# Kernel tuning notes

Measured on AMD Instinct MI355X. Metric: run time of the kernel, lower is better.

## Reference

```python
import jax, jax.numpy as jnp
import numpy as np

NUM_SLOTS = 4096
NUM_CLUSTER = 10
SLOT_DIM = 64
EPS = 1e-8
N_ITER = 3
LN_EPS = 1e-5


def _ln(x, g, b):
    m = jnp.mean(x, axis=-1, keepdims=True)
    v = jnp.var(x, axis=-1, keepdims=True)
    return (x - m) / jnp.sqrt(v + LN_EPS) * g + b


def setup_inputs() -> dict:
    key = jax.random.key(0)
    ks = jax.random.split(key, 24)
    d, S = SLOT_DIM, NUM_SLOTS
    s = d ** -0.5
    f32 = jnp.float32
    return {
        "cluster_centers": jax.random.normal(ks[0], (NUM_CLUSTER, d), f32),
        "Wk": jax.random.normal(ks[1], (d, d), f32) * s,
        "bk": jnp.zeros((d,), f32),
        "Wq": jax.random.normal(ks[2], (d, d), f32) * s,
        "bq": jnp.zeros((d,), f32),
        "Wv": jax.random.normal(ks[3], (d, d), f32) * s,
        "bv": jnp.zeros((d,), f32),
        "cc_g": jnp.ones((d,), f32),
        "cc_b": jnp.zeros((d,), f32),
        "W_ih": jax.random.normal(ks[4], (3 * d, d), f32) * s,
        "W_hh": jax.random.normal(ks[5], (3 * d, d), f32) * s,
        "b_ih": jnp.zeros((3 * d,), f32),
        "b_hh": jnp.zeros((3 * d,), f32),
        "ln_g": jnp.ones((d,), f32),
        "ln_b": jnp.zeros((d,), f32),
        "W1": jax.random.normal(ks[6], (2 * d, d), f32) * s,
        "b1": jnp.zeros((2 * d,), f32),
        "W2": jax.random.normal(ks[7], (d, 2 * d), f32) * (2 * d) ** -0.5,
        "b2": jnp.zeros((d,), f32),
        "Wa": jax.random.normal(ks[8], (S, d, d), f32) * s,
        "ba": jnp.zeros((S, d), f32),
        "Wb": jax.random.normal(ks[9], (S, d, d), f32) * s,
        "bb": jnp.zeros((S, d), f32),
    }


def reference(cluster_centers, Wk, bk, Wq, bq, Wv, bv, cc_g, cc_b,
              W_ih, W_hh, b_ih, b_hh, ln_g, ln_b, W1, b1, W2, b2,
              Wa, ba, Wb, bb):
    temp = SLOT_DIM ** -0.5
    k = cluster_centers @ Wk.T + bk          # [N, d]
    v = cluster_centers @ Wv.T + bv          # [N, d]
    cc = cluster_centers
    for _ in range(N_ITER):
        cc_prev = cc
        q = _ln(cc, cc_g, cc_b) @ Wq.T + bq  # [N, d]
        attn = jnp.einsum('nd,md->nm', k, q) * temp
        attn = jax.nn.softmax(attn, axis=0) + EPS
        attn = attn / jnp.sum(attn, axis=-1, keepdims=True)
        updates = attn @ v                   # [N, d]
        # PyTorch GRUCell
        gi = updates @ W_ih.T + b_ih
        gh = cc_prev @ W_hh.T + b_hh
        ir, iz, inn = jnp.split(gi, 3, axis=-1)
        hr, hz, hn = jnp.split(gh, 3, axis=-1)
        r = jax.nn.sigmoid(ir + hr)
        z = jax.nn.sigmoid(iz + hz)
        n = jnp.tanh(inn + r * hn)
        cc = (1.0 - z) * n + z * cc_prev
        # residual MLP
        h = _ln(cc, ln_g, ln_b)
        cc = cc + jax.nn.relu(h @ W1.T + b1) @ W2.T + b2
    # per-slot 2-layer MLP + max over the 10 clusters, vectorized over slots
    h = jax.nn.relu(jnp.einsum('sij,nj->sni', Wa, cc) + ba[:, None, :])  # [S, N, d]
    out = jnp.einsum('sij,snj->sni', Wb, h) + bb[:, None, :]             # [S, N, d]
    return jnp.max(out, axis=1)                                          # [S, d]
```

## Files before the change

### kernel.cpp

```cpp
#include <hip/hip_runtime.h>
#include <math.h>

#define NCLU 10
#define D    64
#define NSLOT 4096

typedef unsigned int   u32;
typedef unsigned short u16;

typedef __attribute__((ext_vector_type(8))) short  bf16x8;
typedef __attribute__((ext_vector_type(4))) float  f32x4;

__device__ __forceinline__ u16 f2bf_rne(float f) {
    u32 u = __float_as_uint(f);
    return (u16)((u + 0x7fffu + ((u >> 16) & 1u)) >> 16);
}

__device__ __forceinline__ bf16x8 pack8(float4 a, float4 b) {
    bf16x8 r;
    r[0] = (short)f2bf_rne(a.x); r[1] = (short)f2bf_rne(a.y);
    r[2] = (short)f2bf_rne(a.z); r[3] = (short)f2bf_rne(a.w);
    r[4] = (short)f2bf_rne(b.x); r[5] = (short)f2bf_rne(b.y);
    r[6] = (short)f2bf_rne(b.z); r[7] = (short)f2bf_rne(b.w);
    return r;
}

__device__ __forceinline__ float wred(float v) {
#pragma unroll
    for (int off = 32; off > 0; off >>= 1) v += __shfl_xor(v, off);
    return v;
}

__device__ __forceinline__ void load_afrags64(bf16x8 a[4][2], const float* __restrict__ W,
                                              int lc, int quad) {
#pragma unroll
    for (int mt = 0; mt < 4; ++mt)
#pragma unroll
        for (int kt = 0; kt < 2; ++kt) {
            const float* p = W + (16 * mt + lc) * 64 + kt * 32 + quad * 8;
            a[mt][kt] = pack8(*(const float4*)p, *(const float4*)(p + 4));
        }
}

__device__ __forceinline__ void load_afrags128(bf16x8 a[4][2], const float* __restrict__ W,
                                               int ktbase, int lc, int quad) {
#pragma unroll
    for (int mt = 0; mt < 4; ++mt)
#pragma unroll
        for (int kt = 0; kt < 2; ++kt) {
            const float* p = W + (16 * mt + lc) * 128 + (ktbase + kt) * 32 + quad * 8;
            a[mt][kt] = pack8(*(const float4*)p, *(const float4*)(p + 4));
        }
}

__device__ __forceinline__ bf16x8 bfrag(const float* __restrict__ xbase, int xstride,
                                        int lc, int quad, int ktglob) {
    if (lc < NCLU) {
        const float* p = xbase + lc * xstride + ktglob * 32 + quad * 8;
        return pack8(*(const float4*)p, *(const float4*)(p + 4));
    }
    bf16x8 z;
#pragma unroll
    for (int j = 0; j < 8; ++j) z[j] = 0;
    return z;
}

__device__ __forceinline__ void mm_apply(const bf16x8 a[4][2], const float* __restrict__ xbase,
                                         int xstride, int ktbase,
                                         float* __restrict__ obase, int ostride, int ooff,
                                         const float* __restrict__ bias, bool do_relu,
                                         int lc, int quad) {
    f32x4 acc[4];
#pragma unroll
    for (int mt = 0; mt < 4; ++mt) acc[mt] = (f32x4){0.f, 0.f, 0.f, 0.f};
#pragma unroll
    for (int kt = 0; kt < 2; ++kt) {
        bf16x8 b = bfrag(xbase, xstride, lc, quad, ktbase + kt);
#pragma unroll
        for (int mt = 0; mt < 4; ++mt)
            acc[mt] = __builtin_amdgcn_mfma_f32_16x16x32_bf16(a[mt][kt], b, acc[mt], 0, 0, 0);
    }
    if (lc < NCLU) {
#pragma unroll
        for (int mt = 0; mt < 4; ++mt) {
            float4 o;
            o.x = acc[mt][0]; o.y = acc[mt][1]; o.z = acc[mt][2]; o.w = acc[mt][3];
            if (bias) {
                float4 bv = *(const float4*)(bias + 16 * mt + 4 * quad);
                o.x += bv.x; o.y += bv.y; o.z += bv.z; o.w += bv.w;
            }
            if (do_relu) {
                o.x = fmaxf(o.x, 0.f); o.y = fmaxf(o.y, 0.f);
                o.z = fmaxf(o.z, 0.f); o.w = fmaxf(o.w, 0.f);
            }
            *(float4*)(obase + lc * ostride + ooff + 16 * mt + 4 * quad) = o;
        }
    }
}

__global__ __launch_bounds__(640, 3) void phase1_kernel(
    const float* __restrict__ cc0,
    const float* __restrict__ Wk, const float* __restrict__ bk,
    const float* __restrict__ Wq, const float* __restrict__ bq,
    const float* __restrict__ Wv, const float* __restrict__ bv,
    const float* __restrict__ cc_g, const float* __restrict__ cc_b,
    const float* __restrict__ W_ih, const float* __restrict__ W_hh,
    const float* __restrict__ b_ih, const float* __restrict__ b_hh,
    const float* __restrict__ ln_g, const float* __restrict__ ln_b,
    const float* __restrict__ W1, const float* __restrict__ b1,
    const float* __restrict__ W2, const float* __restrict__ b2,
    float* __restrict__ cc_out)
{
    const int t = threadIdx.x;
    const int w = t >> 6;
    const int i = t & 63;
    const int quad = i >> 4;
    const int lc   = i & 15;

    __shared__ float ccl[NCLU][68];
    __shared__ float xl[NCLU][68];
    __shared__ float kl[NCLU][68];
    __shared__ float vl[NCLU][68];
    __shared__ float ql[NCLU][68];
    __shared__ float ul[NCLU][68];
    __shared__ float hl[NCLU][68];
    __shared__ float dl9[NCLU][68];
    __shared__ float dl8[NCLU][68];
    __shared__ float tl[NCLU][132];
    __shared__ float gl[6][NCLU][68];
    __shared__ float al[NCLU][12];

    const float g_cc = cc_g[i], b_cc = cc_b[i];
    const float g_ln = ln_g[i], b_ln = ln_b[i];

    bf16x8 afrA[4][2], afrB[4][2];
#pragma unroll
    for (int mt = 0; mt < 4; ++mt)
#pragma unroll
        for (int kt = 0; kt < 2; ++kt) {
#pragma unroll
            for (int j = 0; j < 8; ++j) { afrA[mt][kt][j] = 0; afrB[mt][kt][j] = 0; }
        }

    const float* biasA = nullptr;
    if (w == 0)      { load_afrags64(afrA, Wq, lc, quad);                    biasA = bq; }
    else if (w <= 3) { load_afrags64(afrA, W_ih + (w - 1) * 64 * 64, lc, quad); biasA = b_ih + (w - 1) * 64; }
    else if (w <= 6) { load_afrags64(afrA, W_hh + (w - 4) * 64 * 64, lc, quad); biasA = b_hh + (w - 4) * 64; }
    else if (w == 7) { load_afrags64(afrA, Wk, lc, quad); }
    else if (w == 8) { load_afrags64(afrA, Wv, lc, quad);
                       load_afrags128(afrB, W2, 2, lc, quad); }
    else             { load_afrags128(afrA, W2, 0, lc, quad); biasA = b2; }

    float c = cc0[w * 64 + i];
    ccl[w][i] = c;
    __syncthreads();

    if (w == 7)      mm_apply(afrA, &ccl[0][0], 68, 0, &kl[0][0], 68, 0, bk, false, lc, quad);
    else if (w == 8) mm_apply(afrA, &ccl[0][0], 68, 0, &vl[0][0], 68, 0, bv, false, lc, quad);
    __syncthreads();

    if (w == 7)      { load_afrags64(afrA, W1, lc, quad);            biasA = b1; }
    else if (w == 8) { load_afrags64(afrA, W1 + 64 * 64, lc, quad);  biasA = b1 + 64; }

    for (int it = 0; it < 3; ++it) {
        {
            float s1 = wred(c), s2 = wred(c * c);
            float mu = s1 * (1.f / 64.f);
            float va = s2 * (1.f / 64.f) - mu * mu;
            xl[w][i] = (c - mu) * rsqrtf(va + 1e-5f) * g_cc + b_cc;
        }
        __syncthreads();

        if (w == 0)
            mm_apply(afrA, &xl[0][0], 68, 0, &ql[0][0], 68, 0, biasA, false, lc, quad);
        else if (w >= 4 && w <= 6)
            mm_apply(afrA, &ccl[0][0], 68, 0, &gl[w - 1][0][0], 68, 0, biasA, false, lc, quad);
        __syncthreads();

        if (i < NCLU) {
            const float4* kf = (const float4*)&kl[w][0];
            const float4* qf = (const float4*)&ql[i][0];
            float a0 = 0.f, a1 = 0.f, a2 = 0.f, a3 = 0.f;
#pragma unroll
            for (int jj = 0; jj < 16; ++jj) {
                float4 kv = kf[jj], qv = qf[jj];
                a0 += kv.x * qv.x; a1 += kv.y * qv.y; a2 += kv.z * qv.z; a3 += kv.w * qv.w;
            }
            al[w][i] = ((a0 + a1) + (a2 + a3)) * 0.125f;
        }
        __syncthreads();

        if (t < NCLU) {
            float mx = -1e30f;
#pragma unroll
            for (int nn = 0; nn < NCLU; ++nn) mx = fmaxf(mx, al[nn][t]);
            float e[NCLU]; float s = 0.f;
#pragma unroll
            for (int nn = 0; nn < NCLU; ++nn) { e[nn] = __expf(al[nn][t] - mx); s += e[nn]; }
            float inv = 1.f / s;
#pragma unroll
            for (int nn = 0; nn < NCLU; ++nn) al[nn][t] = e[nn] * inv + 1e-8f;
        }
        __syncthreads();
        if (t < NCLU) {
            float s = 0.f;
#pragma unroll
            for (int m = 0; m < NCLU; ++m) s += al[t][m];
            float inv = 1.f / s;
#pragma unroll
            for (int m = 0; m < NCLU; ++m) al[t][m] *= inv;
        }
        __syncthreads();

        {
            float u = 0.f;
#pragma unroll
            for (int m = 0; m < NCLU; ++m) u += al[w][m] * vl[m][i];
            ul[w][i] = u;
        }
        __syncthreads();

        if (w >= 1 && w <= 3)
            mm_apply(afrA, &ul[0][0], 68, 0, &gl[w - 1][0][0], 68, 0, biasA, false, lc, quad);
        __syncthreads();

        {
            float ir = gl[0][w][i], iz = gl[1][w][i], inn = gl[2][w][i];
            float hr = gl[3][w][i], hz = gl[4][w][i], hn = gl[5][w][i];
            float r = 1.f / (1.f + __expf(-(ir + hr)));
            float z = 1.f / (1.f + __expf(-(iz + hz)));
            float nn2 = tanhf(inn + r * hn);
            c = (1.f - z) * nn2 + z * c;

            float s1 = wred(c), s2 = wred(c * c);
            float mu = s1 * (1.f / 64.f);
            float va = s2 * (1.f / 64.f) - mu * mu;
            hl[w][i] = (c - mu) * rsqrtf(va + 1e-5f) * g_ln + b_ln;
        }
        __syncthreads();

        if (w == 7)
            mm_apply(afrA, &hl[0][0], 68, 0, &tl[0][0], 132, 0, biasA, true, lc, quad);
        else if (w == 8)
            mm_apply(afrA, &hl[0][0], 68, 0, &tl[0][0], 132, 64, biasA, true, lc, quad);
        __syncthreads();

        if (w == 9)
            mm_apply(afrA, &tl[0][0], 132, 0, &dl9[0][0], 68, 0, biasA, false, lc, quad);
        else if (w == 8)
            mm_apply(afrB, &tl[0][0], 132, 2, &dl8[0][0], 68, 0, nullptr, false, lc, quad);
        __syncthreads();

        c += dl9[w][i] + dl8[w][i];
        ccl[w][i] = c;
        __syncthreads();
    }

    cc_out[w * 64 + i] = c;
}

#define HSTR 72
__global__ __launch_bounds__(64, 4) void phase2_kernel(
    const float* __restrict__ Wa, const float* __restrict__ ba,
    const float* __restrict__ Wb, const float* __restrict__ bb,
    const float* __restrict__ cc, float* __restrict__ out)
{
    const int s = blockIdx.x;
    const int l = threadIdx.x;
    const int quad = l >> 4;
    const int lc   = l & 15;

    __shared__ u16 hT[16 * HSTR];

    const float* wa = Wa + (size_t)s * 4096;
    const float* wb = Wb + (size_t)s * 4096;

    bf16x8 bcc[2];
#pragma unroll
    for (int kt = 0; kt < 2; ++kt) {
        if (lc < NCLU) {
            const float* cp = cc + lc * 64 + kt * 32 + quad * 8;
            bcc[kt] = pack8(*(const float4*)cp, *(const float4*)(cp + 4));
        } else {
#pragma unroll
            for (int j = 0; j < 8; ++j) bcc[kt][j] = 0;
        }
    }

    float4 rg[16];
#pragma unroll
    for (int mt = 0; mt < 4; ++mt)
#pragma unroll
        for (int kt = 0; kt < 2; ++kt) {
            const float* p = wa + (16 * mt + lc) * 64 + kt * 32 + quad * 8;
            rg[(mt * 2 + kt) * 2 + 0] = *(const float4*)p;
            rg[(mt * 2 + kt) * 2 + 1] = *(const float4*)(p + 4);
        }

    bf16x8 frA[4][2];
#pragma unroll
    for (int mt = 0; mt < 4; ++mt)
#pragma unroll
        for (int kt = 0; kt < 2; ++kt)
            frA[mt][kt] = pack8(rg[(mt * 2 + kt) * 2], rg[(mt * 2 + kt) * 2 + 1]);

#pragma unroll
    for (int mt = 0; mt < 4; ++mt)
#pragma unroll
        for (int kt = 0; kt < 2; ++kt) {
            const float* p = wb + (16 * mt + lc) * 64 + kt * 32 + quad * 8;
            rg[(mt * 2 + kt) * 2 + 0] = *(const float4*)p;
            rg[(mt * 2 + kt) * 2 + 1] = *(const float4*)(p + 4);
        }

    f32x4 acc[4];
#pragma unroll
    for (int mt = 0; mt < 4; ++mt) acc[mt] = (f32x4){0.f, 0.f, 0.f, 0.f};
#pragma unroll
    for (int kt = 0; kt < 2; ++kt)
#pragma unroll
        for (int mt = 0; mt < 4; ++mt)
            acc[mt] = __builtin_amdgcn_mfma_f32_16x16x32_bf16(frA[mt][kt], bcc[kt], acc[mt], 0, 0, 0);

#pragma unroll
    for (int mt = 0; mt < 4; ++mt) {
        float4 bav = *(const float4*)(ba + s * 64 + 16 * mt + quad * 4);
        u16 h0 = f2bf_rne(fmaxf(acc[mt][0] + bav.x, 0.f));
        u16 h1 = f2bf_rne(fmaxf(acc[mt][1] + bav.y, 0.f));
        u16 h2 = f2bf_rne(fmaxf(acc[mt][2] + bav.z, 0.f));
        u16 h3 = f2bf_rne(fmaxf(acc[mt][3] + bav.w, 0.f));
        uint2 pk; pk.x = (u32)h0 | ((u32)h1 << 16); pk.y = (u32)h2 | ((u32)h3 << 16);
        *(uint2*)(&hT[lc * HSTR + 16 * mt + quad * 4]) = pk;
    }

    bf16x8 frB[4][2];
#pragma unroll
    for (int mt = 0; mt < 4; ++mt)
#pragma unroll
        for (int kt = 0; kt < 2; ++kt)
            frB[mt][kt] = pack8(rg[(mt * 2 + kt) * 2], rg[(mt * 2 + kt) * 2 + 1]);

    bf16x8 bh[2];
#pragma unroll
    for (int kt = 0; kt < 2; ++kt)
        bh[kt] = *(const bf16x8*)(&hT[lc * HSTR + kt * 32 + quad * 8]);

    f32x4 acc2[4];
#pragma unroll
    for (int mt = 0; mt < 4; ++mt) acc2[mt] = (f32x4){0.f, 0.f, 0.f, 0.f};
#pragma unroll
    for (int kt = 0; kt < 2; ++kt)
#pragma unroll
        for (int mt = 0; mt < 4; ++mt)
            acc2[mt] = __builtin_amdgcn_mfma_f32_16x16x32_bf16(frB[mt][kt], bh[kt], acc2[mt], 0, 0, 0);

    const float NEG = -3.0e38f;
#pragma unroll
    for (int mt = 0; mt < 4; ++mt) {
#pragma unroll
        for (int r = 0; r < 4; ++r) {
            float v = (lc < NCLU) ? acc2[mt][r] : NEG;
#pragma unroll
            for (int off = 1; off < 16; off <<= 1)
                v = fmaxf(v, __shfl_xor(v, off));
            acc2[mt][r] = v;
        }
    }

    if (lc < 4) {
#pragma unroll
        for (int mt = 0; mt < 4; ++mt) {
            int row = 16 * mt + 4 * quad + lc;
            out[s * 64 + row] = acc2[mt][lc] + bb[s * 64 + row];
        }
    }
}

extern "C" void kernel_launch(void* const* d_in, const int* in_sizes, int n_in,
                              void* d_out, int out_size, void* d_ws, size_t ws_size,
                              hipStream_t stream) {
    const float* cc0  = (const float*)d_in[0];
    const float* Wk   = (const float*)d_in[1];
    const float* bk   = (const float*)d_in[2];
    const float* Wq   = (const float*)d_in[3];
    const float* bq   = (const float*)d_in[4];
    const float* Wv   = (const float*)d_in[5];
    const float* bv   = (const float*)d_in[6];
    const float* ccg  = (const float*)d_in[7];
    const float* ccb  = (const float*)d_in[8];
    const float* Wih  = (const float*)d_in[9];
    const float* Whh  = (const float*)d_in[10];
    const float* bih  = (const float*)d_in[11];
    const float* bhh  = (const float*)d_in[12];
    const float* lng  = (const float*)d_in[13];
    const float* lnb  = (const float*)d_in[14];
    const float* W1   = (const float*)d_in[15];
    const float* b1   = (const float*)d_in[16];
    const float* W2   = (const float*)d_in[17];
    const float* b2   = (const float*)d_in[18];
    const float* Wa   = (const float*)d_in[19];
    const float* ba   = (const float*)d_in[20];
    const float* Wb   = (const float*)d_in[21];
    const float* bb   = (const float*)d_in[22];

    float* cc_ws = (float*)d_ws;
    float* out   = (float*)d_out;

    hipLaunchKernelGGL(phase1_kernel, dim3(1), dim3(640), 0, stream,
                       cc0, Wk, bk, Wq, bq, Wv, bv, ccg, ccb,
                       Wih, Whh, bih, bhh, lng, lnb, W1, b1, W2, b2, cc_ws);

    hipLaunchKernelGGL(phase2_kernel, dim3(NSLOT), dim3(64), 0, stream,
                       Wa, ba, Wb, bb, cc_ws, out);
}
```

Baseline: 216.8 us.

## Pack four slots per block and issue all weight loads before conversion

The phase2 kernel now runs four waves per block, one slot each, with a private shared-memory tile per wave, so the grid shrinks to a quarter of its former block count. The Wa, Wb and bias loads are all issued up front into separate register arrays before any bf16 packing, so more global memory traffic is in flight per wave. The cost is higher register pressure (32 float4 staging registers), which may limit occupancy under the new launch bounds.

Measured after the change: 218.5 us. Within noise of the previous version (+0.8%).

```diff
diff --git a/kernel.cpp b/kernel.cpp
--- a/kernel.cpp
+++ b/kernel.cpp
@@ -260,17 +260,19 @@
 }
 
 #define HSTR 72
-__global__ __launch_bounds__(64, 4) void phase2_kernel(
+#define SLOTS_PER_BLK 4
+__global__ __launch_bounds__(256, 4) void phase2_kernel(
     const float* __restrict__ Wa, const float* __restrict__ ba,
     const float* __restrict__ Wb, const float* __restrict__ bb,
     const float* __restrict__ cc, float* __restrict__ out)
 {
-    const int s = blockIdx.x;
-    const int l = threadIdx.x;
+    const int w = threadIdx.x >> 6;
+    const int l = threadIdx.x & 63;
+    const int s = blockIdx.x * SLOTS_PER_BLK + w;
     const int quad = l >> 4;
     const int lc   = l & 15;
 
-    __shared__ u16 hT[16 * HSTR];
+    __shared__ u16 hT[SLOTS_PER_BLK][16 * HSTR];
 
     const float* wa = Wa + (size_t)s * 4096;
     const float* wb = Wb + (size_t)s * 4096;
@@ -287,31 +289,37 @@
         }
     }
 
-    float4 rg[16];
+    float4 bav[4];
+#pragma unroll
+    for (int mt = 0; mt < 4; ++mt)
+        bav[mt] = *(const float4*)(ba + s * 64 + 16 * mt + quad * 4);
+
+    float4 rgA[16];
 #pragma unroll
     for (int mt = 0; mt < 4; ++mt)
 #pragma unroll
         for (int kt = 0; kt < 2; ++kt) {
             const float* p = wa + (16 * mt + lc) * 64 + kt * 32 + quad * 8;
-            rg[(mt * 2 + kt) * 2 + 0] = *(const float4*)p;
-            rg[(mt * 2 + kt) * 2 + 1] = *(const float4*)(p + 4);
-        }
-
-    bf16x8 frA[4][2];
-#pragma unroll
-    for (int mt = 0; mt < 4; ++mt)
-#pragma unroll
-        for (int kt = 0; kt < 2; ++kt)
-            frA[mt][kt] = pack8(rg[(mt * 2 + kt) * 2], rg[(mt * 2 + kt) * 2 + 1]);
-
+            rgA[(mt * 2 + kt) * 2 + 0] = *(const float4*)p;
+            rgA[(mt * 2 + kt) * 2 + 1] = *(const float4*)(p + 4);
+        }
+
+    float4 rgB[16];
 #pragma unroll
     for (int mt = 0; mt < 4; ++mt)
 #pragma unroll
         for (int kt = 0; kt < 2; ++kt) {
             const float* p = wb + (16 * mt + lc) * 64 + kt * 32 + quad * 8;
-            rg[(mt * 2 + kt) * 2 + 0] = *(const float4*)p;
-            rg[(mt * 2 + kt) * 2 + 1] = *(const float4*)(p + 4);
-        }
+            rgB[(mt * 2 + kt) * 2 + 0] = *(const float4*)p;
+            rgB[(mt * 2 + kt) * 2 + 1] = *(const float4*)(p + 4);
+        }
+
+    bf16x8 frA[4][2];
+#pragma unroll
+    for (int mt = 0; mt < 4; ++mt)
+#pragma unroll
+        for (int kt = 0; kt < 2; ++kt)
+            frA[mt][kt] = pack8(rgA[(mt * 2 + kt) * 2], rgA[(mt * 2 + kt) * 2 + 1]);
 
     f32x4 acc[4];
 #pragma unroll
@@ -324,13 +332,12 @@
 
 #pragma unroll
     for (int mt = 0; mt < 4; ++mt) {
-        float4 bav = *(const float4*)(ba + s * 64 + 16 * mt + quad * 4);
-        u16 h0 = f2bf_rne(fmaxf(acc[mt][0] + bav.x, 0.f));
-        u16 h1 = f2bf_rne(fmaxf(acc[mt][1] + bav.y, 0.f));
-        u16 h2 = f2bf_rne(fmaxf(acc[mt][2] + bav.z, 0.f));
-        u16 h3 = f2bf_rne(fmaxf(acc[mt][3] + bav.w, 0.f));
+        u16 h0 = f2bf_rne(fmaxf(acc[mt][0] + bav[mt].x, 0.f));
+        u16 h1 = f2bf_rne(fmaxf(acc[mt][1] + bav[mt].y, 0.f));
+        u16 h2 = f2bf_rne(fmaxf(acc[mt][2] + bav[mt].z, 0.f));
+        u16 h3 = f2bf_rne(fmaxf(acc[mt][3] + bav[mt].w, 0.f));
         uint2 pk; pk.x = (u32)h0 | ((u32)h1 << 16); pk.y = (u32)h2 | ((u32)h3 << 16);
-        *(uint2*)(&hT[lc * HSTR + 16 * mt + quad * 4]) = pk;
+        *(uint2*)(&hT[w][lc * HSTR + 16 * mt + quad * 4]) = pk;
     }
 
     bf16x8 frB[4][2];
@@ -338,12 +345,12 @@
     for (int mt = 0; mt < 4; ++mt)
 #pragma unroll
         for (int kt = 0; kt < 2; ++kt)
-            frB[mt][kt] = pack8(rg[(mt * 2 + kt) * 2], rg[(mt * 2 + kt) * 2 + 1]);
+            frB[mt][kt] = pack8(rgB[(mt * 2 + kt) * 2], rgB[(mt * 2 + kt) * 2 + 1]);
 
     bf16x8 bh[2];
 #pragma unroll
     for (int kt = 0; kt < 2; ++kt)
-        bh[kt] = *(const bf16x8*)(&hT[lc * HSTR + kt * 32 + quad * 8]);
+        bh[kt] = *(const bf16x8*)(&hT[w][lc * HSTR + kt * 32 + quad * 8]);
 
     f32x4 acc2[4];
 #pragma unroll
@@ -410,6 +417,6 @@
                        cc0, Wk, bk, Wq, bq, Wv, bv, ccg, ccb,
                        Wih, Whh, bih, bhh, lng, lnb, W1, b1, W2, b2, cc_ws);
 
-    hipLaunchKernelGGL(phase2_kernel, dim3(NSLOT), dim3(64), 0, stream,
+    hipLaunchKernelGGL(phase2_kernel, dim3(NSLOT / SLOTS_PER_BLK), dim3(256), 0, stream,
                        Wa, ba, Wb, bb, cc_ws, out);
 }
```

## Split phase2 per-slot MLP across four waves, one 16-row tile each

Applied to the files above, without the earlier changes.

Phase2 now launches 256 threads per slot instead of 64. Each wavefront owns one 16-row M-tile of Wa and Wb, and the waves share the hidden activations through LDS with a block barrier. All Wa and Wb loads are issued up front so each wave keeps more memory requests in flight and uses fewer registers. The cost is a __syncthreads per block and redundant loads of cc across the four waves.

Result: no change. 214.4 us (median of 2 runs) (-1.1%).

```diff
diff --git a/kernel.cpp b/kernel.cpp
--- a/kernel.cpp
+++ b/kernel.cpp
@@ -260,13 +260,14 @@
 }
 
 #define HSTR 72
-__global__ __launch_bounds__(64, 4) void phase2_kernel(
+__global__ __launch_bounds__(256, 5) void phase2_kernel(
     const float* __restrict__ Wa, const float* __restrict__ ba,
     const float* __restrict__ Wb, const float* __restrict__ bb,
     const float* __restrict__ cc, float* __restrict__ out)
 {
+    const int w = threadIdx.x >> 6;
+    const int l = threadIdx.x & 63;
     const int s = blockIdx.x;
-    const int l = threadIdx.x;
     const int quad = l >> 4;
     const int lc   = l & 15;
 
@@ -275,104 +276,83 @@
     const float* wa = Wa + (size_t)s * 4096;
     const float* wb = Wb + (size_t)s * 4096;
 
+    float4 c00, c01, c10, c11;
+    if (lc < NCLU) {
+        const float* cp = cc + lc * 64;
+        c00 = *(const float4*)(cp + 0 * 32 + quad * 8);
+        c01 = *(const float4*)(cp + 0 * 32 + quad * 8 + 4);
+        c10 = *(const float4*)(cp + 1 * 32 + quad * 8);
+        c11 = *(const float4*)(cp + 1 * 32 + quad * 8 + 4);
+    }
+    float4 a00, a01, a10, a11;
+    {
+        const float* p0 = wa + (16 * w + lc) * 64 + 0 * 32 + quad * 8;
+        const float* p1 = wa + (16 * w + lc) * 64 + 1 * 32 + quad * 8;
+        a00 = *(const float4*)p0; a01 = *(const float4*)(p0 + 4);
+        a10 = *(const float4*)p1; a11 = *(const float4*)(p1 + 4);
+    }
+    float4 bav = *(const float4*)(ba + s * 64 + 16 * w + quad * 4);
+    float4 b00, b01, b10, b11;
+    {
+        const float* p0 = wb + (16 * w + lc) * 64 + 0 * 32 + quad * 8;
+        const float* p1 = wb + (16 * w + lc) * 64 + 1 * 32 + quad * 8;
+        b00 = *(const float4*)p0; b01 = *(const float4*)(p0 + 4);
+        b10 = *(const float4*)p1; b11 = *(const float4*)(p1 + 4);
+    }
+
+    bf16x8 frA[2];
+    frA[0] = pack8(a00, a01);
+    frA[1] = pack8(a10, a11);
     bf16x8 bcc[2];
-#pragma unroll
-    for (int kt = 0; kt < 2; ++kt) {
-        if (lc < NCLU) {
-            const float* cp = cc + lc * 64 + kt * 32 + quad * 8;
-            bcc[kt] = pack8(*(const float4*)cp, *(const float4*)(cp + 4));
-        } else {
-#pragma unroll
-            for (int j = 0; j < 8; ++j) bcc[kt][j] = 0;
-        }
-    }
-
-    float4 rg[16];
-#pragma unroll
-    for (int mt = 0; mt < 4; ++mt)
-#pragma unroll
-        for (int kt = 0; kt < 2; ++kt) {
-            const float* p = wa + (16 * mt + lc) * 64 + kt * 32 + quad * 8;
-            rg[(mt * 2 + kt) * 2 + 0] = *(const float4*)p;
-            rg[(mt * 2 + kt) * 2 + 1] = *(const float4*)(p + 4);
-        }
-
-    bf16x8 frA[4][2];
-#pragma unroll
-    for (int mt = 0; mt < 4; ++mt)
-#pragma unroll
-        for (int kt = 0; kt < 2; ++kt)
-            frA[mt][kt] = pack8(rg[(mt * 2 + kt) * 2], rg[(mt * 2 + kt) * 2 + 1]);
-
-#pragma unroll
-    for (int mt = 0; mt < 4; ++mt)
-#pragma unroll
-        for (int kt = 0; kt < 2; ++kt) {
-            const float* p = wb + (16 * mt + lc) * 64 + kt * 32 + quad * 8;
-            rg[(mt * 2 + kt) * 2 + 0] = *(const float4*)p;
-            rg[(mt * 2 + kt) * 2 + 1] = *(const float4*)(p + 4);
-        }
-
-    f32x4 acc[4];
-#pragma unroll
-    for (int mt = 0; mt < 4; ++mt) acc[mt] = (f32x4){0.f, 0.f, 0.f, 0.f};
-#pragma unroll
-    for (int kt = 0; kt < 2; ++kt)
-#pragma unroll
-        for (int mt = 0; mt < 4; ++mt)
-            acc[mt] = __builtin_amdgcn_mfma_f32_16x16x32_bf16(frA[mt][kt], bcc[kt], acc[mt], 0, 0, 0);
-
-#pragma unroll
-    for (int mt = 0; mt < 4; ++mt) {
-        float4 bav = *(const float4*)(ba + s * 64 + 16 * mt + quad * 4);
-        u16 h0 = f2bf_rne(fmaxf(acc[mt][0] + bav.x, 0.f));
-        u16 h1 = f2bf_rne(fmaxf(acc[mt][1] + bav.y, 0.f));
-        u16 h2 = f2bf_rne(fmaxf(acc[mt][2] + bav.z, 0.f));
-        u16 h3 = f2bf_rne(fmaxf(acc[mt][3] + bav.w, 0.f));
+    if (lc < NCLU) {
+        bcc[0] = pack8(c00, c01);
+        bcc[1] = pack8(c10, c11);
+    } else {
+#pragma unroll
+        for (int j = 0; j < 8; ++j) { bcc[0][j] = 0; bcc[1][j] = 0; }
+    }
+
+    f32x4 acc = (f32x4){0.f, 0.f, 0.f, 0.f};
+    acc = __builtin_amdgcn_mfma_f32_16x16x32_bf16(frA[0], bcc[0], acc, 0, 0, 0);
+    acc = __builtin_amdgcn_mfma_f32_16x16x32_bf16(frA[1], bcc[1], acc, 0, 0, 0);
+
+    {
+        u16 h0 = f2bf_rne(fmaxf(acc[0] + bav.x, 0.f));
+        u16 h1 = f2bf_rne(fmaxf(acc[1] + bav.y, 0.f));
+        u16 h2 = f2bf_rne(fmaxf(acc[2] + bav.z, 0.f));
+        u16 h3 = f2bf_rne(fmaxf(acc[3] + bav.w, 0.f));
         uint2 pk; pk.x = (u32)h0 | ((u32)h1 << 16); pk.y = (u32)h2 | ((u32)h3 << 16);
-        *(uint2*)(&hT[lc * HSTR + 16 * mt + quad * 4]) = pk;
-    }
-
-    bf16x8 frB[4][2];
-#pragma unroll
-    for (int mt = 0; mt < 4; ++mt)
-#pragma unroll
-        for (int kt = 0; kt < 2; ++kt)
-            frB[mt][kt] = pack8(rg[(mt * 2 + kt) * 2], rg[(mt * 2 + kt) * 2 + 1]);
+        *(uint2*)(&hT[lc * HSTR + 16 * w + quad * 4]) = pk;
+    }
+
+    bf16x8 frB[2];
+    frB[0] = pack8(b00, b01);
+    frB[1] = pack8(b10, b11);
+
+    __syncthreads();
 
     bf16x8 bh[2];
 #pragma unroll
     for (int kt = 0; kt < 2; ++kt)
         bh[kt] = *(const bf16x8*)(&hT[lc * HSTR + kt * 32 + quad * 8]);
 
-    f32x4 acc2[4];
-#pragma unroll
-    for (int mt = 0; mt < 4; ++mt) acc2[mt] = (f32x4){0.f, 0.f, 0.f, 0.f};
-#pragma unroll
-    for (int kt = 0; kt < 2; ++kt)
-#pragma unroll
-        for (int mt = 0; mt < 4; ++mt)
-            acc2[mt] = __builtin_amdgcn_mfma_f32_16x16x32_bf16(frB[mt][kt], bh[kt], acc2[mt], 0, 0, 0);
+    f32x4 acc2 = (f32x4){0.f, 0.f, 0.f, 0.f};
+    acc2 = __builtin_amdgcn_mfma_f32_16x16x32_bf16(frB[0], bh[0], acc2, 0, 0, 0);
+    acc2 = __builtin_amdgcn_mfma_f32_16x16x32_bf16(frB[1], bh[1], acc2, 0, 0, 0);
 
     const float NEG = -3.0e38f;
 #pragma unroll
-    for (int mt = 0; mt < 4; ++mt) {
-#pragma unroll
-        for (int r = 0; r < 4; ++r) {
-            float v = (lc < NCLU) ? acc2[mt][r] : NEG;
-#pragma unroll
-            for (int off = 1; off < 16; off <<= 1)
-                v = fmaxf(v, __shfl_xor(v, off));
-            acc2[mt][r] = v;
-        }
+    for (int r = 0; r < 4; ++r) {
+        float v = (lc < NCLU) ? acc2[r] : NEG;
+#pragma unroll
+        for (int off = 1; off < 16; off <<= 1)
+            v = fmaxf(v, __shfl_xor(v, off));
+        acc2[r] = v;
     }
 
     if (lc < 4) {
-#pragma unroll
-        for (int mt = 0; mt < 4; ++mt) {
-            int row = 16 * mt + 4 * quad + lc;
-            out[s * 64 + row] = acc2[mt][lc] + bb[s * 64 + row];
-        }
+        int row = 16 * w + 4 * quad + lc;
+        out[s * 64 + row] = acc2[lc] + bb[s * 64 + row];
     }
 }
 
@@ -410,6 +390,6 @@
                        cc0, Wk, bk, Wq, bq, Wv, bv, ccg, ccb,
                        Wih, Whh, bih, bhh, lng, lnb, W1, b1, W2, b2, cc_ws);
 
-    hipLaunchKernelGGL(phase2_kernel, dim3(NSLOT), dim3(64), 0, stream,
+    hipLaunchKernelGGL(phase2_kernel, dim3(NSLOT), dim3(256), 0, stream,
                        Wa, ba, Wb, bb, cc_ws, out);
 }
```
